# Kernel optimization log

Measured on AMD Instinct MI355X. Metric: run time of the kernel, lower is better.

## Reference

```python
import jax, jax.numpy as jnp
import numpy as np

N_NODES = 50000
N_EDGES = 1000000
N_QUERY = 100000
NUM_FEATURES = 256
HIDDEN = 256
LABEL_DIM = 2


def glorot(key, shape):
    lim = float(np.sqrt(6.0 / (shape[0] + shape[1])))
    return jax.random.uniform(key, shape, jnp.float32, -lim, lim)


def setup_inputs() -> dict:
    key = jax.random.key(0)
    ks = jax.random.split(key, 8)
    x = jax.random.normal(ks[0], (N_NODES, NUM_FEATURES), jnp.float32)
    edge_index = jax.random.randint(ks[1], (2, N_EDGES), 0, N_NODES)
    query_edges = jax.random.randint(ks[2], (N_QUERY, 2), 0, N_NODES)
    edge_weight = jax.random.uniform(ks[3], (N_EDGES,), jnp.float32)
    W1 = glorot(ks[4], (NUM_FEATURES, HIDDEN))
    b1 = jnp.zeros((HIDDEN,), jnp.float32)
    W2 = glorot(ks[5], (HIDDEN, HIDDEN))
    b2 = jnp.zeros((HIDDEN,), jnp.float32)
    Wl = glorot(ks[6], (2 * HIDDEN, LABEL_DIM))
    bl = jnp.zeros((LABEL_DIM,), jnp.float32)
    return {"x": x, "edge_index": edge_index, "query_edges": query_edges,
            "edge_weight": edge_weight, "W1": W1, "b1": b1, "W2": W2,
            "b2": b2, "Wl": Wl, "bl": bl}


def digcn_conv(x, edge_index, edge_weight, W, b):
    # x: [N, F_in] -> h: [N, F_out]; propagate: out[dst] += w_e * h[src]
    h = x @ W
    src, dst = edge_index[0], edge_index[1]
    msg = h[src] * edge_weight[:, None]            # [E, F_out]
    agg = jax.ops.segment_sum(msg, dst, num_segments=x.shape[0])
    return agg + b


def reference(x, edge_index, query_edges, edge_weight, W1, b1, W2, b2, Wl, bl):
    h = jax.nn.relu(digcn_conv(x, edge_index, edge_weight, W1, b1))
    # dropout is identity at eval time
    h = digcn_conv(h, edge_index, edge_weight, W2, b2)
    q = jnp.concatenate((h[query_edges[:, 0]], h[query_edges[:, 1]]), axis=-1)
    logits = q @ Wl + bl
    return jax.nn.log_softmax(logits, axis=1)
```

## Files before the change

### kernel.cpp

```cpp
#include <hip/hip_runtime.h>
#include <hip/hip_bf16.h>
#include <math.h>

typedef __bf16 bf16;
typedef __bf16 v8bf __attribute__((ext_vector_type(8)));
typedef __bf16 v4bf __attribute__((ext_vector_type(4)));
typedef float  v4f  __attribute__((ext_vector_type(4)));

#define FDIM 256
#define BKT_CAP 8192
#define AROW 264
#define GEMM_BLOCKS 352
#define K3_BLOCKS 512
#define P3_BLOCKS (K3_BLOCKS - GEMM_BLOCKS)


__global__ __launch_bounds__(256) void flag_kernel(float* __restrict__ out, int n) {
  int i = blockIdx.x * 256 + threadIdx.x;
  if (i < n) out[i] = 1.0e9f;
}

__global__ __launch_bounds__(256) void k1_prep(const float* __restrict__ W1,
                                               const float* __restrict__ W2,
                                               bf16* __restrict__ Wt1,
                                               const int* __restrict__ dst,
                                               int* __restrict__ phist,
                                               const float* __restrict__ Wl,
                                               const float* __restrict__ b2,
                                               const float* __restrict__ bl,
                                               float4* __restrict__ V,
                                               float* __restrict__ cc,
                                               int E, int N, int nbkt) {
  __shared__ int h[256];
  __shared__ float sWl[1024];
  __shared__ float red[256];
  int b = blockIdx.x;
  int t = threadIdx.x;
  if (b < 256) {
    int k = b;
    Wt1[t * FDIM + k] = (bf16)W1[k * FDIM + t];
  } else if (b < 512) {
    int pb = b - 256;
    h[t] = 0;
    __syncthreads();
    for (int e = pb * 256 + t; e < E; e += 256 * 256) {
      int d = dst[e];
      d = d < 0 ? 0 : (d >= N ? N - 1 : d);
      atomicAdd(&h[d >> 8], 1);
    }
    __syncthreads();
    phist[pb * 256 + t] = h[t];
  } else {
#pragma unroll
    for (int j = 0; j < 4; ++j) sWl[j * 256 + t] = Wl[j * 256 + t];
    __syncthreads();
    const float* w2row = W2 + (size_t)t * FDIM;
    float4 acc = make_float4(0.f, 0.f, 0.f, 0.f);
    for (int j = 0; j < 256; ++j) {
      float w = w2row[j];
      acc.x += w * sWl[2 * j + 0];
      acc.y += w * sWl[2 * j + 1];
      acc.z += w * sWl[512 + 2 * j + 0];
      acc.w += w * sWl[512 + 2 * j + 1];
    }
    V[t] = acc;
    float bj = b2[t];
    red[t] = bj * (sWl[2 * t + 0] + sWl[512 + 2 * t + 0]);
    __syncthreads();
    if (t == 0) {
      float s = 0.f;
      for (int j = 0; j < 256; ++j) s += red[j];
      cc[0] = s + bl[0];
    }
    __syncthreads();
    red[t] = bj * (sWl[2 * t + 1] + sWl[512 + 2 * t + 1]);
    __syncthreads();
    if (t == 0) {
      float s = 0.f;
      for (int j = 0; j < 256; ++j) s += red[j];
      cc[1] = s + bl[1];
    }
  }
}

__global__ __launch_bounds__(256) void p2_scan(const int* __restrict__ phist,
                                               int* __restrict__ bbase,
                                               int* __restrict__ gcur,
                                               int* __restrict__ offs,
                                               int nbkt, int Nn) {
  __shared__ int wsum[4];
  int t = threadIdx.x, lane = t & 63, wv = t >> 6;
  int v = 0;
  for (int pb = 0; pb < 256; ++pb) v += phist[pb * 256 + t];
  if (t >= nbkt) v = 0;
  int x = v;
#pragma unroll
  for (int d = 1; d < 64; d <<= 1) {
    int y = __shfl_up(x, d, 64);
    if (lane >= d) x += y;
  }
  if (lane == 63) wsum[wv] = x;
  __syncthreads();
  int woff = 0;
  if (wv >= 1) woff += wsum[0];
  if (wv >= 2) woff += wsum[1];
  if (wv >= 3) woff += wsum[2];
  int incl = woff + x;
  int excl = incl - v;
  if (t < nbkt) { bbase[t] = excl; gcur[t] = excl; }
  if (t == 255) {
    bbase[nbkt] = incl;
    offs[Nn] = incl;
  }
}


__device__ inline void stage64(const float* __restrict__ A, bf16* __restrict__ As,
                               int row0, int M, int tid) {
#pragma unroll
  for (int j = 0; j < 8; ++j) {
    int g = j * 2048 + tid * 8;
    int r = g >> 8, c = g & 255;
    int gr = row0 + r; if (gr >= M) gr = M - 1;
    const float* p = A + (size_t)gr * FDIM + c;
    float4 f0 = *reinterpret_cast<const float4*>(p);
    float4 f1 = *reinterpret_cast<const float4*>(p + 4);
    v8bf o;
    o[0] = (bf16)f0.x; o[1] = (bf16)f0.y; o[2] = (bf16)f0.z; o[3] = (bf16)f0.w;
    o[4] = (bf16)f1.x; o[5] = (bf16)f1.y; o[6] = (bf16)f1.z; o[7] = (bf16)f1.w;
    *reinterpret_cast<v8bf*>(As + r * AROW + c) = o;
  }
}

__device__ inline void gemm_body(const float* __restrict__ A, const bf16* __restrict__ Bt,
                                 bf16* __restrict__ C, int M, int bid, int nblocks,
                                 bf16* __restrict__ As) {
  const int K = FDIM, N = FDIM;
  int tid = threadIdx.x;
  int wave = tid >> 6;
  int lane = tid & 63;
  int l15 = lane & 15, quad = lane >> 4;

  v8bf bfr[4][8];
#pragma unroll
  for (int nn = 0; nn < 4; ++nn) {
    const bf16* bp = Bt + (size_t)(wave * 64 + nn * 16 + l15) * K + quad * 8;
#pragma unroll
    for (int kk = 0; kk < 8; ++kk)
      bfr[nn][kk] = *reinterpret_cast<const v8bf*>(bp + kk * 32);
  }

  int ntiles = (M + 63) >> 6;
  for (int tile = bid; tile < ntiles; tile += nblocks) {
    int row0 = tile * 64;
    __syncthreads();
    stage64(A, As, row0, M, tid);
    __syncthreads();

#pragma unroll
    for (int st = 0; st < 4; ++st) {
      v8bf afr[8];
#pragma unroll
      for (int kk = 0; kk < 8; ++kk)
        afr[kk] = *reinterpret_cast<const v8bf*>(As + (st * 16 + l15) * AROW + quad * 8 + kk * 32);

      v4f acc[4];
#pragma unroll
      for (int nn = 0; nn < 4; ++nn) acc[nn] = (v4f){0.f, 0.f, 0.f, 0.f};

#pragma unroll
      for (int kk = 0; kk < 8; ++kk)
#pragma unroll
        for (int nn = 0; nn < 4; ++nn)
          acc[nn] = __builtin_amdgcn_mfma_f32_16x16x32_bf16(afr[kk], bfr[nn][kk], acc[nn], 0, 0, 0);

#pragma unroll
      for (int nn = 0; nn < 4; ++nn)
#pragma unroll
        for (int r = 0; r < 4; ++r) {
          int row = row0 + st * 16 + quad * 4 + r;
          int col = wave * 64 + nn * 16 + l15;
          if (row < M) C[(size_t)row * N + col] = (bf16)acc[nn][r];
        }
    }
  }
}

__device__ inline void p3_body(const int* __restrict__ src, const int* __restrict__ dst,
                               const float* __restrict__ ew, int* __restrict__ gcur,
                               uint2* __restrict__ tmp, int E, int N, int nbkt,
                               int pb, int nblocks, int* h, int* base, int* cnt) {
  int t = threadIdx.x;
  int chunk = (E + nblocks - 1) / nblocks;
  int lo = pb * chunk;
  int hi = lo + chunk; if (hi > E) hi = E;
  h[t] = 0; cnt[t] = 0;
  __syncthreads();
  for (int e = lo + t; e < hi; e += 256) {
    int d = dst[e];
    d = d < 0 ? 0 : (d >= N ? N - 1 : d);
    atomicAdd(&h[d >> 8], 1);
  }
  __syncthreads();
  if (t < nbkt) base[t] = atomicAdd(&gcur[t], h[t]);
  __syncthreads();
  for (int e = lo + t; e < hi; e += 256) {
    int d = dst[e];
    d = d < 0 ? 0 : (d >= N ? N - 1 : d);
    int b = d >> 8;
    int sv = src[e];
    sv = sv < 0 ? 0 : (sv >= N ? N - 1 : sv);
    unsigned int u = __float_as_uint(ew[e]);
    unsigned int wbits = ((u + 0x7FFFu + ((u >> 16) & 1u)) & 0xFFFF0000u);
    unsigned int meta = wbits | (unsigned int)(sv & 0xFFFF);
    int r = atomicAdd(&cnt[b], 1);
    int pos = base[b] + r;
    if (pos >= 0 && pos < E) tmp[pos] = make_uint2(meta, (unsigned int)d);
  }
}

__global__ __launch_bounds__(256, 2) void k3_gemm1_p3(const float* __restrict__ x,
                                                      const bf16* __restrict__ Wt1,
                                                      bf16* __restrict__ bufT, int M,
                                                      const int* __restrict__ src,
                                                      const int* __restrict__ dst,
                                                      const float* __restrict__ ew,
                                                      int* __restrict__ gcur,
                                                      uint2* __restrict__ tmp,
                                                      int E, int N, int nbkt) {
  __shared__ bf16 As[64 * AROW];
  __shared__ int h[256], base[256], cnt[256];
  if (blockIdx.x < GEMM_BLOCKS)
    gemm_body(x, Wt1, bufT, M, blockIdx.x, GEMM_BLOCKS, As);
  else
    p3_body(src, dst, ew, gcur, tmp, E, N, nbkt, blockIdx.x - GEMM_BLOCKS, P3_BLOCKS,
            h, base, cnt);
}

__global__ __launch_bounds__(256) void p4_sort(const uint2* __restrict__ tmp,
                                               const int* __restrict__ bbase,
                                               unsigned int* __restrict__ pmeta,
                                               int* __restrict__ offs,
                                               int Nn, int E) {
  __shared__ uint2 ent[BKT_CAP];
  __shared__ int h2[256], ex2[256], c2[256];
  __shared__ int wsum[4];
  int b = blockIdx.x, t = threadIdx.x, lane = t & 63, wv = t >> 6;
  int s0 = bbase[b], s1 = bbase[b + 1];
  int count = s1 - s0;
  if (count < 0) count = 0;
  if (count > BKT_CAP) count = BKT_CAP;
  for (int i = t; i < count; i += 256) ent[i] = tmp[s0 + i];
  h2[t] = 0; c2[t] = 0;
  __syncthreads();
  for (int i = t; i < count; i += 256) atomicAdd(&h2[ent[i].y & 255u], 1);
  __syncthreads();
  int v = h2[t];
  int x = v;
#pragma unroll
  for (int d = 1; d < 64; d <<= 1) {
    int y = __shfl_up(x, d, 64);
    if (lane >= d) x += y;
  }
  if (lane == 63) wsum[wv] = x;
  __syncthreads();
  int woff = 0;
  if (wv >= 1) woff += wsum[0];
  if (wv >= 2) woff += wsum[1];
  if (wv >= 3) woff += wsum[2];
  int excl = woff + x - v;
  ex2[t] = excl;
  int node = (b << 8) + t;
  if (node < Nn) offs[node] = s0 + excl;
  __syncthreads();
  for (int i = t; i < count; i += 256) {
    int l = (int)(ent[i].y & 255u);
    int r = atomicAdd(&c2[l], 1);
    int pos = s0 + ex2[l] + r;
    if (pos >= 0 && pos < E) pmeta[pos] = ent[i].x;
  }
}

__global__ __launch_bounds__(256) void agg1G(const bf16* __restrict__ T,
                                             const unsigned int* __restrict__ pmeta,
                                             const int* __restrict__ offsets,
                                             const float* __restrict__ bias,
                                             const float4* __restrict__ V,
                                             float4* __restrict__ G, int N, int E) {
  int wid = blockIdx.x * 4 + (threadIdx.x >> 6);
  int nw = gridDim.x * 4;
  int lane = threadIdx.x & 63;
  int f = lane * 4;
  const bf16* Tf = T + f;

  float4 bb = *reinterpret_cast<const float4*>(bias + f);
  float4 v0 = V[f + 0], v1 = V[f + 1], v2 = V[f + 2], v3 = V[f + 3];

  for (int node = wid; node < N; node += nw) {
    int nb = __builtin_amdgcn_readfirstlane(node);
    int beg = offsets[nb], end = offsets[nb + 1];
    beg = beg < 0 ? 0 : (beg > E ? E : beg);
    end = end < beg ? beg : (end > E ? E : end);
    int cnt = end - beg;
    const unsigned int* m = pmeta + beg;

    float a0 = 0.f, a1 = 0.f, a2 = 0.f, a3 = 0.f;
    int p = 0;
    for (; p + 8 <= cnt; p += 8) {
      unsigned int mv0 = m[p + 0], mv1 = m[p + 1], mv2 = m[p + 2], mv3 = m[p + 3];
      unsigned int mv4 = m[p + 4], mv5 = m[p + 5], mv6 = m[p + 6], mv7 = m[p + 7];
      v4bf t0 = *reinterpret_cast<const v4bf*>(Tf + ((size_t)(mv0 & 0xFFFFu) << 8));
      v4bf t1 = *reinterpret_cast<const v4bf*>(Tf + ((size_t)(mv1 & 0xFFFFu) << 8));
      v4bf t2 = *reinterpret_cast<const v4bf*>(Tf + ((size_t)(mv2 & 0xFFFFu) << 8));
      v4bf t3 = *reinterpret_cast<const v4bf*>(Tf + ((size_t)(mv3 & 0xFFFFu) << 8));
      v4bf t4 = *reinterpret_cast<const v4bf*>(Tf + ((size_t)(mv4 & 0xFFFFu) << 8));
      v4bf t5 = *reinterpret_cast<const v4bf*>(Tf + ((size_t)(mv5 & 0xFFFFu) << 8));
      v4bf t6 = *reinterpret_cast<const v4bf*>(Tf + ((size_t)(mv6 & 0xFFFFu) << 8));
      v4bf t7 = *reinterpret_cast<const v4bf*>(Tf + ((size_t)(mv7 & 0xFFFFu) << 8));
      float w0 = __uint_as_float(mv0 & 0xFFFF0000u);
      float w1 = __uint_as_float(mv1 & 0xFFFF0000u);
      float w2 = __uint_as_float(mv2 & 0xFFFF0000u);
      float w3 = __uint_as_float(mv3 & 0xFFFF0000u);
      float w4 = __uint_as_float(mv4 & 0xFFFF0000u);
      float w5 = __uint_as_float(mv5 & 0xFFFF0000u);
      float w6 = __uint_as_float(mv6 & 0xFFFF0000u);
      float w7 = __uint_as_float(mv7 & 0xFFFF0000u);
      a0 += w0 * (float)t0[0]; a1 += w0 * (float)t0[1]; a2 += w0 * (float)t0[2]; a3 += w0 * (float)t0[3];
      a0 += w1 * (float)t1[0]; a1 += w1 * (float)t1[1]; a2 += w1 * (float)t1[2]; a3 += w1 * (float)t1[3];
      a0 += w2 * (float)t2[0]; a1 += w2 * (float)t2[1]; a2 += w2 * (float)t2[2]; a3 += w2 * (float)t2[3];
      a0 += w3 * (float)t3[0]; a1 += w3 * (float)t3[1]; a2 += w3 * (float)t3[2]; a3 += w3 * (float)t3[3];
      a0 += w4 * (float)t4[0]; a1 += w4 * (float)t4[1]; a2 += w4 * (float)t4[2]; a3 += w4 * (float)t4[3];
      a0 += w5 * (float)t5[0]; a1 += w5 * (float)t5[1]; a2 += w5 * (float)t5[2]; a3 += w5 * (float)t5[3];
      a0 += w6 * (float)t6[0]; a1 += w6 * (float)t6[1]; a2 += w6 * (float)t6[2]; a3 += w6 * (float)t6[3];
      a0 += w7 * (float)t7[0]; a1 += w7 * (float)t7[1]; a2 += w7 * (float)t7[2]; a3 += w7 * (float)t7[3];
    }
    for (; p < cnt; ++p) {
      unsigned int mv = m[p];
      float w = __uint_as_float(mv & 0xFFFF0000u);
      v4bf tv = *reinterpret_cast<const v4bf*>(Tf + ((size_t)(mv & 0xFFFFu) << 8));
      a0 += w * (float)tv[0];
      a1 += w * (float)tv[1];
      a2 += w * (float)tv[2];
      a3 += w * (float)tv[3];
    }

    float r0 = fmaxf(a0 + bb.x, 0.f);
    float r1 = fmaxf(a1 + bb.y, 0.f);
    float r2 = fmaxf(a2 + bb.z, 0.f);
    float r3 = fmaxf(a3 + bb.w, 0.f);

    float gx = r0 * v0.x + r1 * v1.x + r2 * v2.x + r3 * v3.x;
    float gy = r0 * v0.y + r1 * v1.y + r2 * v2.y + r3 * v3.y;
    float gz = r0 * v0.z + r1 * v1.z + r2 * v2.z + r3 * v3.z;
    float gw = r0 * v0.w + r1 * v1.w + r2 * v2.w + r3 * v3.w;
#pragma unroll
    for (int d = 32; d > 0; d >>= 1) {
      gx += __shfl_down(gx, d, 64);
      gy += __shfl_down(gy, d, 64);
      gz += __shfl_down(gz, d, 64);
      gw += __shfl_down(gw, d, 64);
    }
    if (lane == 0) G[node] = make_float4(gx, gy, gz, gw);
  }
}

__global__ __launch_bounds__(256) void aggP(const float4* __restrict__ G,
                                            const unsigned int* __restrict__ pmeta,
                                            const int* __restrict__ offsets,
                                            float4* __restrict__ P, int N, int E) {
  int node = blockIdx.x * 256 + threadIdx.x;
  if (node >= N) return;
  int beg = offsets[node], end = offsets[node + 1];
  beg = beg < 0 ? 0 : (beg > E ? E : beg);
  end = end < beg ? beg : (end > E ? E : end);
  float ax = 0.f, ay = 0.f, az = 0.f, aw = 0.f;
  int p = beg;
  for (; p + 4 <= end; p += 4) {
    unsigned int m0 = pmeta[p + 0], m1 = pmeta[p + 1], m2 = pmeta[p + 2], m3 = pmeta[p + 3];
    int s0 = (int)(m0 & 0xFFFFu); s0 = s0 >= N ? N - 1 : s0;
    int s1 = (int)(m1 & 0xFFFFu); s1 = s1 >= N ? N - 1 : s1;
    int s2 = (int)(m2 & 0xFFFFu); s2 = s2 >= N ? N - 1 : s2;
    int s3 = (int)(m3 & 0xFFFFu); s3 = s3 >= N ? N - 1 : s3;
    float4 g0 = G[s0], g1 = G[s1], g2 = G[s2], g3 = G[s3];
    float w0 = __uint_as_float(m0 & 0xFFFF0000u);
    float w1 = __uint_as_float(m1 & 0xFFFF0000u);
    float w2 = __uint_as_float(m2 & 0xFFFF0000u);
    float w3 = __uint_as_float(m3 & 0xFFFF0000u);
    ax += w0 * g0.x + w1 * g1.x + w2 * g2.x + w3 * g3.x;
    ay += w0 * g0.y + w1 * g1.y + w2 * g2.y + w3 * g3.y;
    az += w0 * g0.z + w1 * g1.z + w2 * g2.z + w3 * g3.z;
    aw += w0 * g0.w + w1 * g1.w + w2 * g2.w + w3 * g3.w;
  }
  for (; p < end; ++p) {
    unsigned int mm = pmeta[p];
    int s = (int)(mm & 0xFFFFu); s = s >= N ? N - 1 : s;
    float w = __uint_as_float(mm & 0xFFFF0000u);
    float4 g = G[s];
    ax += w * g.x; ay += w * g.y; az += w * g.z; aw += w * g.w;
  }
  P[node] = make_float4(ax, ay, az, aw);
}

__global__ __launch_bounds__(256) void query_small(const int* __restrict__ qe,
                                                   const float4* __restrict__ P,
                                                   const float* __restrict__ cc,
                                                   float* __restrict__ out, int Q, int N) {
  int q = blockIdx.x * 256 + threadIdx.x;
  if (q >= Q) return;
  int n0 = qe[2 * q + 0]; n0 = n0 < 0 ? 0 : (n0 >= N ? N - 1 : n0);
  int n1 = qe[2 * q + 1]; n1 = n1 < 0 ? 0 : (n1 >= N ? N - 1 : n1);
  float4 p0 = P[n0];
  float4 p1 = P[n1];
  float l0 = p0.x + p1.z + cc[0];
  float l1 = p0.y + p1.w + cc[1];
  float m = fmaxf(l0, l1);
  float lse = m + logf(expf(l0 - m) + expf(l1 - m));
  out[2 * q + 0] = l0 - lse;
  out[2 * q + 1] = l1 - lse;
}


extern "C" void kernel_launch(void* const* d_in, const int* in_sizes, int n_in,
                              void* d_out, int out_size, void* d_ws, size_t ws_size,
                              hipStream_t stream) {
  const float* x  = (const float*)d_in[0];
  const int*   ei = (const int*)d_in[1];
  const int*   qe = (const int*)d_in[2];
  const float* ew = (const float*)d_in[3];
  const float* W1 = (const float*)d_in[4];
  const float* b1 = (const float*)d_in[5];
  const float* W2 = (const float*)d_in[6];
  const float* b2 = (const float*)d_in[7];
  const float* Wl = (const float*)d_in[8];
  const float* bl = (const float*)d_in[9];

  int N = in_sizes[0] / FDIM;
  int E = in_sizes[1] / 2;
  int Q = in_sizes[2] / 2;
  const int* srcv = ei;
  const int* dstv = ei + E;
  int nbkt = (N + 255) >> 8;

  size_t off = 0;
  auto alloc = [&](size_t bytes) -> void* {
    void* p = (char*)d_ws + off;
    off += (bytes + 255) & ~(size_t)255;
    return p;
  };
  bf16* bufT  = (bf16*)alloc((size_t)N * FDIM * 2);
  uint2* tmp  = (uint2*)alloc((size_t)E * 8);
  bf16* Wt1   = (bf16*)alloc((size_t)FDIM * FDIM * 2);
  int* offs   = (int*)alloc((size_t)(N + 1) * 4);
  unsigned int* pmeta = (unsigned int*)alloc((size_t)E * 4);
  float4* G   = (float4*)alloc((size_t)N * 16);
  float4* P   = (float4*)alloc((size_t)N * 16);
  float4* V   = (float4*)alloc(256 * 16);
  float* cc   = (float*)alloc(2 * 4);
  int* phist  = (int*)alloc(256 * 256 * 4);
  int* bbase  = (int*)alloc(257 * 4);
  int* gcur   = (int*)alloc(256 * 4);

  if (off > ws_size) {
    flag_kernel<<<(out_size + 255) / 256, 256, 0, stream>>>((float*)d_out, out_size);
    return;
  }

  k1_prep<<<513, 256, 0, stream>>>(W1, W2, Wt1, dstv, phist, Wl, b2, bl, V, cc,
                                   E, N, nbkt);
  p2_scan<<<1, 256, 0, stream>>>(phist, bbase, gcur, offs, nbkt, N);
  k3_gemm1_p3<<<K3_BLOCKS, 256, 0, stream>>>(x, Wt1, bufT, N,
                                             srcv, dstv, ew, gcur, tmp, E, N, nbkt);
  p4_sort<<<nbkt, 256, 0, stream>>>(tmp, bbase, pmeta, offs, N, E);

  agg1G<<<2048, 256, 0, stream>>>(bufT, pmeta, offs, b1, V, G, N, E);

  aggP<<<(N + 255) / 256, 256, 0, stream>>>(G, pmeta, offs, P, N, E);

  query_small<<<(Q + 255) / 256, 256, 0, stream>>>(qe, P, cc, (float*)d_out, Q, N);
}
```

Measured before the change: 249.4 us.

## Split GEMM1 across two fused launches, split agg1G, parallelize aggP per node

The first GEMM is split so its first tiles run alongside bucket scatter (p3) and the remaining tiles run in a new kernel fused with the per-bucket sort (p4), sharing shared memory through a union. The intent is to hide the sort behind GEMM work instead of running it as a separate launch. agg1G is launched twice over node halves with half the grid each, and aggP now uses 4 lanes per node with shuffle reductions to raise parallelism on the gather. The extra launches add overhead, and the shared-memory union enlarges the fused kernel's footprint, which may cut its occupancy.

Measured after the change: 276.7 us. +11.0%, slower.

```diff
diff --git a/kernel.cpp b/kernel.cpp
--- a/kernel.cpp
+++ b/kernel.cpp
@@ -13,6 +13,7 @@
 #define GEMM_BLOCKS 352
 #define K3_BLOCKS 512
 #define P3_BLOCKS (K3_BLOCKS - GEMM_BLOCKS)
+#define GEMM2_BLOCKS 256
 
 
 __global__ __launch_bounds__(256) void flag_kernel(float* __restrict__ out, int n) {
@@ -134,7 +135,7 @@
 
 __device__ inline void gemm_body(const float* __restrict__ A, const bf16* __restrict__ Bt,
                                  bf16* __restrict__ C, int M, int bid, int nblocks,
-                                 bf16* __restrict__ As) {
+                                 bf16* __restrict__ As, int tile_lo, int tile_hi) {
   const int K = FDIM, N = FDIM;
   int tid = threadIdx.x;
   int wave = tid >> 6;
@@ -150,8 +151,7 @@
       bfr[nn][kk] = *reinterpret_cast<const v8bf*>(bp + kk * 32);
   }
 
-  int ntiles = (M + 63) >> 6;
-  for (int tile = bid; tile < ntiles; tile += nblocks) {
+  for (int tile = tile_lo + bid; tile < tile_hi; tile += nblocks) {
     int row0 = tile * 64;
     __syncthreads();
     stage64(A, As, row0, M, tid);
@@ -219,33 +219,13 @@
   }
 }
 
-__global__ __launch_bounds__(256, 2) void k3_gemm1_p3(const float* __restrict__ x,
-                                                      const bf16* __restrict__ Wt1,
-                                                      bf16* __restrict__ bufT, int M,
-                                                      const int* __restrict__ src,
-                                                      const int* __restrict__ dst,
-                                                      const float* __restrict__ ew,
-                                                      int* __restrict__ gcur,
-                                                      uint2* __restrict__ tmp,
-                                                      int E, int N, int nbkt) {
-  __shared__ bf16 As[64 * AROW];
-  __shared__ int h[256], base[256], cnt[256];
-  if (blockIdx.x < GEMM_BLOCKS)
-    gemm_body(x, Wt1, bufT, M, blockIdx.x, GEMM_BLOCKS, As);
-  else
-    p3_body(src, dst, ew, gcur, tmp, E, N, nbkt, blockIdx.x - GEMM_BLOCKS, P3_BLOCKS,
-            h, base, cnt);
-}
-
-__global__ __launch_bounds__(256) void p4_sort(const uint2* __restrict__ tmp,
-                                               const int* __restrict__ bbase,
-                                               unsigned int* __restrict__ pmeta,
-                                               int* __restrict__ offs,
-                                               int Nn, int E) {
-  __shared__ uint2 ent[BKT_CAP];
-  __shared__ int h2[256], ex2[256], c2[256];
-  __shared__ int wsum[4];
-  int b = blockIdx.x, t = threadIdx.x, lane = t & 63, wv = t >> 6;
+__device__ inline void p4_body(const uint2* __restrict__ tmp,
+                               const int* __restrict__ bbase,
+                               unsigned int* __restrict__ pmeta,
+                               int* __restrict__ offs,
+                               int Nn, int E, int b,
+                               uint2* ent, int* h2, int* ex2, int* c2, int* wsum) {
+  int t = threadIdx.x, lane = t & 63, wv = t >> 6;
   int s0 = bbase[b], s1 = bbase[b + 1];
   int count = s1 - s0;
   if (count < 0) count = 0;
@@ -281,12 +261,58 @@
   }
 }
 
+__global__ __launch_bounds__(256, 2) void k3a_gemm1_p3(const float* __restrict__ x,
+                                                       const bf16* __restrict__ Wt1,
+                                                       bf16* __restrict__ bufT, int M,
+                                                       const int* __restrict__ src,
+                                                       const int* __restrict__ dst,
+                                                       const float* __restrict__ ew,
+                                                       int* __restrict__ gcur,
+                                                       uint2* __restrict__ tmp,
+                                                       int E, int N, int nbkt,
+                                                       int tile_mid) {
+  __shared__ bf16 As[64 * AROW];
+  __shared__ int h[256], base[256], cnt[256];
+  if (blockIdx.x < GEMM_BLOCKS)
+    gemm_body(x, Wt1, bufT, M, blockIdx.x, GEMM_BLOCKS, As, 0, tile_mid);
+  else
+    p3_body(src, dst, ew, gcur, tmp, E, N, nbkt, blockIdx.x - GEMM_BLOCKS, P3_BLOCKS,
+            h, base, cnt);
+}
+
+struct P4Smem {
+  uint2 ent[BKT_CAP];
+  int h2[256]; int ex2[256]; int c2[256]; int wsum[4];
+};
+union K3bSmem {
+  bf16 As[64 * AROW];
+  P4Smem p4;
+};
+
+__global__ __launch_bounds__(256, 2) void k3b_gemm2_p4(const float* __restrict__ x,
+                                                       const bf16* __restrict__ Wt1,
+                                                       bf16* __restrict__ bufT, int M,
+                                                       const uint2* __restrict__ tmp,
+                                                       const int* __restrict__ bbase,
+                                                       unsigned int* __restrict__ pmeta,
+                                                       int* __restrict__ offs,
+                                                       int E, int Nn,
+                                                       int tile_mid, int ntiles) {
+  __shared__ K3bSmem u;
+  if (blockIdx.x < GEMM2_BLOCKS)
+    gemm_body(x, Wt1, bufT, M, blockIdx.x, GEMM2_BLOCKS, u.As, tile_mid, ntiles);
+  else
+    p4_body(tmp, bbase, pmeta, offs, Nn, E, blockIdx.x - GEMM2_BLOCKS,
+            u.p4.ent, u.p4.h2, u.p4.ex2, u.p4.c2, u.p4.wsum);
+}
+
 __global__ __launch_bounds__(256) void agg1G(const bf16* __restrict__ T,
                                              const unsigned int* __restrict__ pmeta,
                                              const int* __restrict__ offsets,
                                              const float* __restrict__ bias,
                                              const float4* __restrict__ V,
-                                             float4* __restrict__ G, int N, int E) {
+                                             float4* __restrict__ G,
+                                             int node_lo, int node_hi, int E, int N) {
   int wid = blockIdx.x * 4 + (threadIdx.x >> 6);
   int nw = gridDim.x * 4;
   int lane = threadIdx.x & 63;
@@ -296,7 +322,7 @@
   float4 bb = *reinterpret_cast<const float4*>(bias + f);
   float4 v0 = V[f + 0], v1 = V[f + 1], v2 = V[f + 2], v3 = V[f + 3];
 
-  for (int node = wid; node < N; node += nw) {
+  for (int node = node_lo + wid; node < node_hi; node += nw) {
     int nb = __builtin_amdgcn_readfirstlane(node);
     int beg = offsets[nb], end = offsets[nb + 1];
     beg = beg < 0 ? 0 : (beg > E ? E : beg);
@@ -368,37 +394,38 @@
                                             const unsigned int* __restrict__ pmeta,
                                             const int* __restrict__ offsets,
                                             float4* __restrict__ P, int N, int E) {
-  int node = blockIdx.x * 256 + threadIdx.x;
+  int node = blockIdx.x * 64 + (threadIdx.x >> 2);
   if (node >= N) return;
+  int j = threadIdx.x & 3;
   int beg = offsets[node], end = offsets[node + 1];
   beg = beg < 0 ? 0 : (beg > E ? E : beg);
   end = end < beg ? beg : (end > E ? E : end);
   float ax = 0.f, ay = 0.f, az = 0.f, aw = 0.f;
-  int p = beg;
-  for (; p + 4 <= end; p += 4) {
-    unsigned int m0 = pmeta[p + 0], m1 = pmeta[p + 1], m2 = pmeta[p + 2], m3 = pmeta[p + 3];
+  int p = beg + j;
+  for (; p + 4 < end; p += 8) {
+    unsigned int m0 = pmeta[p], m1 = pmeta[p + 4];
     int s0 = (int)(m0 & 0xFFFFu); s0 = s0 >= N ? N - 1 : s0;
     int s1 = (int)(m1 & 0xFFFFu); s1 = s1 >= N ? N - 1 : s1;
-    int s2 = (int)(m2 & 0xFFFFu); s2 = s2 >= N ? N - 1 : s2;
-    int s3 = (int)(m3 & 0xFFFFu); s3 = s3 >= N ? N - 1 : s3;
-    float4 g0 = G[s0], g1 = G[s1], g2 = G[s2], g3 = G[s3];
+    float4 g0 = G[s0], g1 = G[s1];
     float w0 = __uint_as_float(m0 & 0xFFFF0000u);
     float w1 = __uint_as_float(m1 & 0xFFFF0000u);
-    float w2 = __uint_as_float(m2 & 0xFFFF0000u);
-    float w3 = __uint_as_float(m3 & 0xFFFF0000u);
-    ax += w0 * g0.x + w1 * g1.x + w2 * g2.x + w3 * g3.x;
-    ay += w0 * g0.y + w1 * g1.y + w2 * g2.y + w3 * g3.y;
-    az += w0 * g0.z + w1 * g1.z + w2 * g2.z + w3 * g3.z;
-    aw += w0 * g0.w + w1 * g1.w + w2 * g2.w + w3 * g3.w;
-  }
-  for (; p < end; ++p) {
+    ax += w0 * g0.x + w1 * g1.x;
+    ay += w0 * g0.y + w1 * g1.y;
+    az += w0 * g0.z + w1 * g1.z;
+    aw += w0 * g0.w + w1 * g1.w;
+  }
+  if (p < end) {
     unsigned int mm = pmeta[p];
     int s = (int)(mm & 0xFFFFu); s = s >= N ? N - 1 : s;
     float w = __uint_as_float(mm & 0xFFFF0000u);
     float4 g = G[s];
     ax += w * g.x; ay += w * g.y; az += w * g.z; aw += w * g.w;
   }
-  P[node] = make_float4(ax, ay, az, aw);
+  ax += __shfl_xor(ax, 1, 64); ax += __shfl_xor(ax, 2, 64);
+  ay += __shfl_xor(ay, 1, 64); ay += __shfl_xor(ay, 2, 64);
+  az += __shfl_xor(az, 1, 64); az += __shfl_xor(az, 2, 64);
+  aw += __shfl_xor(aw, 1, 64); aw += __shfl_xor(aw, 2, 64);
+  if (j == 0) P[node] = make_float4(ax, ay, az, aw);
 }
 
 __global__ __launch_bounds__(256) void query_small(const int* __restrict__ qe,
@@ -440,6 +467,9 @@
   const int* srcv = ei;
   const int* dstv = ei + E;
   int nbkt = (N + 255) >> 8;
+  int ntiles = (N + 63) >> 6;
+  int tile_mid = GEMM_BLOCKS;
+  if (tile_mid > ntiles) tile_mid = ntiles;
 
   size_t off = 0;
   auto alloc = [&](size_t bytes) -> void* {
@@ -468,13 +498,18 @@
   k1_prep<<<513, 256, 0, stream>>>(W1, W2, Wt1, dstv, phist, Wl, b2, bl, V, cc,
                                    E, N, nbkt);
   p2_scan<<<1, 256, 0, stream>>>(phist, bbase, gcur, offs, nbkt, N);
-  k3_gemm1_p3<<<K3_BLOCKS, 256, 0, stream>>>(x, Wt1, bufT, N,
-                                             srcv, dstv, ew, gcur, tmp, E, N, nbkt);
-  p4_sort<<<nbkt, 256, 0, stream>>>(tmp, bbase, pmeta, offs, N, E);
-
-  agg1G<<<2048, 256, 0, stream>>>(bufT, pmeta, offs, b1, V, G, N, E);
-
-  aggP<<<(N + 255) / 256, 256, 0, stream>>>(G, pmeta, offs, P, N, E);
+  k3a_gemm1_p3<<<K3_BLOCKS, 256, 0, stream>>>(x, Wt1, bufT, N,
+                                              srcv, dstv, ew, gcur, tmp, E, N, nbkt,
+                                              tile_mid);
+  k3b_gemm2_p4<<<GEMM2_BLOCKS + nbkt, 256, 0, stream>>>(x, Wt1, bufT, N,
+                                                        tmp, bbase, pmeta, offs, E, N,
+                                                        tile_mid, ntiles);
+
+  int half = (N + 1) >> 1;
+  agg1G<<<1024, 256, 0, stream>>>(bufT, pmeta, offs, b1, V, G, 0, half, E, N);
+  agg1G<<<1024, 256, 0, stream>>>(bufT, pmeta, offs, b1, V, G, half, N, E, N);
+
+  aggP<<<(N * 4 + 255) / 256, 256, 0, stream>>>(G, pmeta, offs, P, N, E);
 
   query_small<<<(Q + 255) / 256, 256, 0, stream>>>(qe, P, cc, (float*)d_out, Q, N);
 }
```
